# Kernel optimization log

Measured on AMD Instinct MI355X. Metric: run time of the kernel, lower is better.

Reference implementation:

```python
import jax, jax.numpy as jnp
import numpy as np

C = 1024            # hidden_dim // compression_rate
IN_DIM = 1024
OUT_DIM = 1024
FFT_LEN = C // 2 + 1
CURV = 1e-4         # self.c
EPS = 1e-7
LN_EPS = 1e-5


def _mobius_scalar_mul(r, x, c):
    # r (x) x = tanh(r * atanh(sqrt(c)||x||)) * x / (sqrt(c)||x||)
    sqrt_c = jnp.sqrt(c)
    norm = jnp.maximum(jnp.linalg.norm(x, axis=-1, keepdims=True), EPS)
    scn = jnp.clip(sqrt_c * norm, EPS, 1.0 - 1e-5)
    return jnp.tanh(r * jnp.arctanh(scn)) * x / (sqrt_c * norm)


def _mobius_add(x, y, c):
    x2 = jnp.sum(x * x, axis=-1, keepdims=True)
    y2 = jnp.sum(y * y, axis=-1, keepdims=True)
    xy = jnp.sum(x * y, axis=-1, keepdims=True)
    num = (1.0 + 2.0 * c * xy + c * y2) * x + (1.0 - c * x2) * y
    den = 1.0 + 2.0 * c * xy + (c * c) * x2 * y2
    return num / jnp.maximum(den, EPS)


def _poincare_ball_layer(u, v, c, t):
    # geodesic-style interpolation: ((1-t) (x) u) (+) (t (x) v)
    return _mobius_add(_mobius_scalar_mul(1.0 - t, u, c),
                       _mobius_scalar_mul(t, v, c), c)


def setup_inputs() -> dict:
    key = jax.random.key(0)
    k_x, k_p, k_d = jax.random.split(key, 3)
    std = 0.02
    x = jax.random.normal(k_x, (4, 2048, IN_DIM), dtype=jnp.float32)
    proj_w = jax.random.normal(k_p, (C, IN_DIM), dtype=jnp.float32) * std
    freq_w = jnp.zeros((FFT_LEN,), dtype=jnp.float32)
    t = jnp.float32(0.3)
    ln_g = jnp.ones((C,), dtype=jnp.float32)
    ln_b = jnp.zeros((C,), dtype=jnp.float32)
    down_w = jax.random.normal(k_d, (OUT_DIM, C), dtype=jnp.float32) * std
    scale = jnp.float32(1.0)
    return {"x": x, "proj_w": proj_w, "ln_g": ln_g, "ln_b": ln_b,
            "freq_w": freq_w, "t": t, "down_w": down_w, "scale": scale}


def reference(x, proj_w, ln_g, ln_b, freq_w, t, down_w, scale):
    B, L, _ = x.shape
    # non-sep branch (hidden_dim > in_dim): silu(Linear(x))
    comp = jax.nn.silu(jnp.einsum('bli,ci->blc', x, proj_w))
    mu = jnp.mean(comp, axis=-1, keepdims=True)
    var = jnp.var(comp, axis=-1, keepdims=True)
    comp = (comp - mu) * jax.lax.rsqrt(var + LN_EPS) * ln_g + ln_b
    comp = comp.reshape(-1, C)                     # [B*L, C]
    Xf = jnp.fft.rfft(comp, axis=1)                # [B*L, C//2+1]
    w = jax.nn.softmax(freq_w)[None, :]
    flat = jnp.fft.irfft(Xf * w, n=C, axis=1)
    flat = jnp.nan_to_num(flat)
    shift = jnp.nan_to_num(t * flat)
    hyp = jnp.nan_to_num(_poincare_ball_layer(flat, shift, CURV, t))
    hyp = hyp.reshape(B, L, C)
    return jnp.einsum('blc,oc->blo', hyp, down_w) * scale
```

## Files before the change

### kernel.cpp

```cpp
#include <hip/hip_runtime.h>
#include <math.h>

typedef float f32x4 __attribute__((ext_vector_type(4)));
typedef __bf16 bf16x8 __attribute__((ext_vector_type(8)));
typedef unsigned short u16x8 __attribute__((ext_vector_type(8)));

__device__ __forceinline__ unsigned short f2bf(float f) {
  unsigned u = __float_as_uint(f);
  unsigned r = (u + 0x7fffu + ((u >> 16) & 1u)) >> 16;
  return (unsigned short)r;
}
__device__ __forceinline__ float bf2f(unsigned short h) {
  return __uint_as_float(((unsigned)h) << 16);
}

__device__ __forceinline__ float blk_sum(float v, float* red, int tid) {
  #pragma unroll
  for (int o = 32; o; o >>= 1) v += __shfl_down(v, o);
  __syncthreads();
  if ((tid & 63) == 0) red[tid >> 6] = v;
  __syncthreads();
  return red[0] + red[1] + red[2] + red[3];
}

__global__ __launch_bounds__(256) void k_s(const float* __restrict__ fw,
                                           float* __restrict__ s,
                                           float* __restrict__ pw) {
  __shared__ float wsh[513];
  __shared__ float red[4];
  int tid = threadIdx.x;
  float m = -1e30f;
  for (int i = tid; i < 513; i += 256) m = fmaxf(m, fw[i]);
  #pragma unroll
  for (int o = 32; o; o >>= 1) m = fmaxf(m, __shfl_down(m, o));
  if ((tid & 63) == 0) red[tid >> 6] = m;
  __syncthreads();
  m = fmaxf(fmaxf(red[0], red[1]), fmaxf(red[2], red[3]));
  float sum = 0.f;
  for (int i = tid; i < 513; i += 256) {
    float e = expf(fw[i] - m);
    wsh[i] = e;
    sum += e;
  }
  sum = blk_sum(sum, red, tid);
  float inv = 1.f / sum;

  if (blockIdx.x == 0) {
    for (int i = tid; i < 513; i += 256) {
      float wn = wsh[i] * inv;
      float cf = (i == 0 || i == 512) ? 1.f : 2.f;
      pw[i] = cf * wn * wn * (1.f / 1024.f);
    }
  }

  int gid = blockIdx.x * 256 + tid;
  int d = gid >> 3;
  int chunk = gid & 7;
  float acc = 0.f;
  for (int f = 1 + chunk; f < 512; f += 8) {
    int p = (f * d) & 1023;
    acc += wsh[f] * __cosf(6.283185307179586f * (float)p * (1.f / 1024.f));
  }
  acc += __shfl_xor(acc, 1);
  acc += __shfl_xor(acc, 2);
  acc += __shfl_xor(acc, 4);
  if (chunk == 0) {
    float tot = wsh[0] + ((d & 1) ? -wsh[512] : wsh[512]) + 2.f * acc;
    s[d] = tot * inv * (1.f / 1024.f);
  }
}

__global__ __launch_bounds__(256) void k_prep(const float* __restrict__ x,
                                              const float* __restrict__ pw,
                                              const float* __restrict__ dw,
                                              const float* __restrict__ s,
                                              unsigned short* __restrict__ xb,
                                              unsigned short* __restrict__ pwb,
                                              unsigned short* __restrict__ dwb,
                                              unsigned short* __restrict__ Sb) {
  int b = blockIdx.x;
  int tid = threadIdx.x;
  if (b < 8192) {
    int i = b * 256 + tid;
    float4 v = ((const float4*)x)[i];
    ushort4 o;
    o.x = f2bf(v.x); o.y = f2bf(v.y); o.z = f2bf(v.z); o.w = f2bf(v.w);
    ((ushort4*)xb)[i] = o;
  } else if (b < 9216) {
    int i = (b - 8192) * 256 + tid;
    float4 v = ((const float4*)pw)[i];
    ushort4 o;
    o.x = f2bf(v.x); o.y = f2bf(v.y); o.z = f2bf(v.z); o.w = f2bf(v.w);
    ((ushort4*)pwb)[i] = o;
  } else if (b < 10240) {
    int i = (b - 9216) * 256 + tid;
    float4 v = ((const float4*)dw)[i];
    ushort4 o;
    o.x = f2bf(v.x); o.y = f2bf(v.y); o.z = f2bf(v.z); o.w = f2bf(v.w);
    ((ushort4*)dwb)[i] = o;
  } else {
    int idx = (b - 10240) * 256 + tid;
    int n = idx >> 8;
    int k0 = (idx & 255) * 4;
    ushort4 o;
    o.x = f2bf(s[(k0 + 0 - n) & 1023]);
    o.y = f2bf(s[(k0 + 1 - n) & 1023]);
    o.z = f2bf(s[(k0 + 2 - n) & 1023]);
    o.w = f2bf(s[(k0 + 3 - n) & 1023]);
    ((ushort4*)Sb)[idx] = o;
  }
}

__device__ __forceinline__ void gemm_body(const unsigned short* __restrict__ A,
                                          const unsigned short* __restrict__ B,
                                          int bm, int bn, int tid,
                                          char* AsB, char* BsB,
                                          f32x4 acc[4][4]) {
  const int lane = tid & 63;
  const int wave = tid >> 6;
  const int mhalf = (wave & 1) * 64;
  const int nhalf = (wave >> 1) * 64;
  const int ar = tid >> 3;
  const int ac = (((tid & 7) ^ (ar & 7))) * 8;
  const unsigned short* Abase = A + (size_t)(bm + ar) * 1024 + ac;
  const unsigned short* Bbase = B + (size_t)(bn + ar) * 1024 + ac;
  const int mrow = lane & 15;
  const int kq = lane >> 4;
  const int sw = mrow & 7;

  for (int kt = 0; kt < 16; ++kt) {
    const int k0 = kt * 64;
    #pragma unroll
    for (int r = 0; r < 4; ++r) {
      __builtin_amdgcn_global_load_lds(
          (const __attribute__((address_space(1))) void*)(Abase + (size_t)(r * 32) * 1024 + k0),
          (__attribute__((address_space(3))) void*)(AsB + r * 4096 + wave * 1024), 16, 0, 0);
      __builtin_amdgcn_global_load_lds(
          (const __attribute__((address_space(1))) void*)(Bbase + (size_t)(r * 32) * 1024 + k0),
          (__attribute__((address_space(3))) void*)(BsB + r * 4096 + wave * 1024), 16, 0, 0);
    }
    __syncthreads();
    #pragma unroll
    for (int kc = 0; kc < 2; ++kc) {
      const int chunk = (kc << 2) | kq;
      bf16x8 af[4], bfr[4];
      #pragma unroll
      for (int mt = 0; mt < 4; ++mt)
        af[mt] = *(const bf16x8*)(AsB + (mhalf + mt * 16 + mrow) * 128 + ((chunk ^ sw) << 4));
      #pragma unroll
      for (int nt = 0; nt < 4; ++nt)
        bfr[nt] = *(const bf16x8*)(BsB + (nhalf + nt * 16 + mrow) * 128 + ((chunk ^ sw) << 4));
      #pragma unroll
      for (int mt = 0; mt < 4; ++mt)
        #pragma unroll
        for (int nt = 0; nt < 4; ++nt)
          acc[mt][nt] = __builtin_amdgcn_mfma_f32_16x16x32_bf16(af[mt], bfr[nt], acc[mt][nt], 0, 0, 0);
    }
    __syncthreads();
  }
}

__global__ __launch_bounds__(256, 5) void k_gemm1w2(const unsigned short* __restrict__ xb,
                                                    const unsigned short* __restrict__ pwb,
                                                    const unsigned short* __restrict__ dwb,
                                                    const unsigned short* __restrict__ Sb,
                                                    unsigned short* __restrict__ comp,
                                                    unsigned short* __restrict__ W2) {
  __shared__ __align__(16) unsigned short As[128 * 64];
  __shared__ __align__(16) unsigned short Bs[64 * 64];
  const int tid = threadIdx.x;
  const int lane = tid & 63;
  const int wave = tid >> 6;
  const int mrow = lane & 15;
  const int kq = lane >> 4;
  const int sw = mrow & 7;
  char* AsB = (char*)As;
  char* BsB = (char*)Bs;

  if (blockIdx.x < 1024) {
    const int gid = blockIdx.x;
    const int xcd = gid & 7;
    const int j = gid >> 3;
    const int ntile = j & 15;
    const int bmIdx = xcd + 8 * (j >> 4);
    const int bm = bmIdx * 128;
    const int bn = ntile * 64;
    const int mhalf = (wave & 1) * 64;
    const int nhalf = (wave >> 1) * 32;
    f32x4 acc[4][2] = {};
    const int ar = tid >> 3;
    const int ac = (((tid & 7) ^ (ar & 7))) * 8;
    const unsigned short* Abase = xb + (size_t)(bm + ar) * 1024 + ac;
    const unsigned short* Bbase = pwb + (size_t)(bn + ar) * 1024 + ac;

    for (int kt = 0; kt < 16; ++kt) {
      const int k0 = kt * 64;
      #pragma unroll
      for (int r = 0; r < 4; ++r)
        __builtin_amdgcn_global_load_lds(
            (const __attribute__((address_space(1))) void*)(Abase + (size_t)(r * 32) * 1024 + k0),
            (__attribute__((address_space(3))) void*)(AsB + r * 4096 + wave * 1024), 16, 0, 0);
      #pragma unroll
      for (int r = 0; r < 2; ++r)
        __builtin_amdgcn_global_load_lds(
            (const __attribute__((address_space(1))) void*)(Bbase + (size_t)(r * 32) * 1024 + k0),
            (__attribute__((address_space(3))) void*)(BsB + r * 4096 + wave * 1024), 16, 0, 0);
      __syncthreads();
      #pragma unroll
      for (int kc = 0; kc < 2; ++kc) {
        const int chunk = (kc << 2) | kq;
        bf16x8 af[4], bfr[2];
        #pragma unroll
        for (int mt = 0; mt < 4; ++mt)
          af[mt] = *(const bf16x8*)(AsB + (mhalf + mt * 16 + mrow) * 128 + ((chunk ^ sw) << 4));
        #pragma unroll
        for (int nt = 0; nt < 2; ++nt)
          bfr[nt] = *(const bf16x8*)(BsB + (nhalf + nt * 16 + mrow) * 128 + ((chunk ^ sw) << 4));
        #pragma unroll
        for (int mt = 0; mt < 4; ++mt)
          #pragma unroll
          for (int nt = 0; nt < 2; ++nt)
            acc[mt][nt] = __builtin_amdgcn_mfma_f32_16x16x32_bf16(af[mt], bfr[nt], acc[mt][nt], 0, 0, 0);
      }
      __syncthreads();
    }

    const int col = bn + nhalf + (lane & 15);
    const int rbase = bm + mhalf + (lane >> 4) * 4;
    #pragma unroll
    for (int mt = 0; mt < 4; ++mt)
      #pragma unroll
      for (int r = 0; r < 4; ++r) {
        const int row = rbase + mt * 16 + r;
        #pragma unroll
        for (int nt = 0; nt < 2; ++nt) {
          float v = acc[mt][nt][r];
          comp[(size_t)row * 1024 + (col + nt * 16)] = f2bf(v / (1.f + expf(-v)));
        }
      }
    return;
  }

  const int wbid = blockIdx.x - 1024;
  const int bm = (wbid >> 4) * 64;
  const int bn = (wbid & 15) * 64;
  const int wm = wave & 1;
  const int wn = wave >> 1;
  f32x4 acc[2][2] = {};
  const int ar = tid >> 3;
  const int ac = (((tid & 7) ^ (ar & 7))) * 8;
  const unsigned short* Abase = dwb + (size_t)(bm + ar) * 1024 + ac;
  const unsigned short* Bbase = Sb + (size_t)(bn + ar) * 1024 + ac;
  for (int kt = 0; kt < 16; ++kt) {
    const int k0 = kt * 64;
    #pragma unroll
    for (int r = 0; r < 2; ++r) {
      __builtin_amdgcn_global_load_lds(
          (const __attribute__((address_space(1))) void*)(Abase + (size_t)(r * 32) * 1024 + k0),
          (__attribute__((address_space(3))) void*)(AsB + r * 4096 + wave * 1024), 16, 0, 0);
      __builtin_amdgcn_global_load_lds(
          (const __attribute__((address_space(1))) void*)(Bbase + (size_t)(r * 32) * 1024 + k0),
          (__attribute__((address_space(3))) void*)(BsB + r * 4096 + wave * 1024), 16, 0, 0);
    }
    __syncthreads();
    #pragma unroll
    for (int kc = 0; kc < 2; ++kc) {
      const int chunk = (kc << 2) | kq;
      bf16x8 af[2], bfr[2];
      #pragma unroll
      for (int mt = 0; mt < 2; ++mt)
        af[mt] = *(const bf16x8*)(AsB + (wm * 32 + mt * 16 + mrow) * 128 + ((chunk ^ sw) << 4));
      #pragma unroll
      for (int nt = 0; nt < 2; ++nt)
        bfr[nt] = *(const bf16x8*)(BsB + (wn * 32 + nt * 16 + mrow) * 128 + ((chunk ^ sw) << 4));
      #pragma unroll
      for (int mt = 0; mt < 2; ++mt)
        #pragma unroll
        for (int nt = 0; nt < 2; ++nt)
          acc[mt][nt] = __builtin_amdgcn_mfma_f32_16x16x32_bf16(af[mt], bfr[nt], acc[mt][nt], 0, 0, 0);
    }
    __syncthreads();
  }
  const int col = bn + wn * 32 + (lane & 15);
  const int rbase = bm + wm * 32 + (lane >> 4) * 4;
  #pragma unroll
  for (int mt = 0; mt < 2; ++mt)
    #pragma unroll
    for (int nt = 0; nt < 2; ++nt)
      #pragma unroll
      for (int r = 0; r < 4; ++r) {
        int row = rbase + mt * 16 + r;
        W2[(size_t)row * 1024 + (col + nt * 16)] = f2bf(acc[mt][nt][r]);
      }
}

#define BFLY(I, J, C, S)                                       \
  {                                                            \
    float tr_ = zr[J] * (C) - zi[J] * (S);                     \
    float ti_ = zr[J] * (S) + zi[J] * (C);                     \
    zr[J] = zr[I] - tr_; zi[J] = zi[I] - ti_;                  \
    zr[I] += tr_;        zi[I] += ti_;                         \
  }

__global__ __launch_bounds__(256) void k_ln(unsigned short* __restrict__ comp,
                                            const float* __restrict__ ln_g,
                                            const float* __restrict__ ln_b,
                                            const float* __restrict__ pw_par,
                                            float* __restrict__ u2) {
  const int tid = threadIdx.x;
  const int lane = tid & 63;
  const int wv = tid >> 6;
  const int row = blockIdx.x * 4 + wv;
  const size_t rowoff = (size_t)row * 1024;
  const int bl = __brev((unsigned)lane) >> 26;
  const int ybase = bl * 16;

  const u16x8* src = (const u16x8*)(comp + rowoff + ybase);
  u16x8 a0 = src[0], a1 = src[1];
  float y[16];
  #pragma unroll
  for (int i = 0; i < 8; ++i) { y[i] = bf2f(a0[i]); y[8 + i] = bf2f(a1[i]); }

  float s1 = 0.f;
  #pragma unroll
  for (int i = 0; i < 16; ++i) s1 += y[i];
  #pragma unroll
  for (int o = 32; o; o >>= 1) s1 += __shfl_xor(s1, o);
  const float mu = s1 * (1.f / 1024.f);
  float s2 = 0.f;
  #pragma unroll
  for (int i = 0; i < 16; ++i) { float d = y[i] - mu; s2 += d * d; }
  #pragma unroll
  for (int o = 32; o; o >>= 1) s2 += __shfl_xor(s2, o);
  const float inv = rsqrtf(s2 * (1.f / 1024.f) + 1e-5f);

  const float4* gp = (const float4*)(ln_g + ybase);
  const float4* bp = (const float4*)(ln_b + ybase);
  #pragma unroll
  for (int q = 0; q < 4; ++q) {
    float4 g = gp[q], b = bp[q];
    y[4 * q + 0] = (y[4 * q + 0] - mu) * inv * g.x + b.x;
    y[4 * q + 1] = (y[4 * q + 1] - mu) * inv * g.y + b.y;
    y[4 * q + 2] = (y[4 * q + 2] - mu) * inv * g.z + b.z;
    y[4 * q + 3] = (y[4 * q + 3] - mu) * inv * g.w + b.w;
  }
  u16x8 o0, o1;
  #pragma unroll
  for (int i = 0; i < 8; ++i) { o0[i] = f2bf(y[i]); o1[i] = f2bf(y[8 + i]); }
  u16x8* dst = (u16x8*)(comp + rowoff + ybase);
  dst[0] = o0; dst[1] = o1;

  float zr[8], zi[8];
  const int cmap[8] = {0, 4, 2, 6, 1, 5, 3, 7};
  #pragma unroll
  for (int r = 0; r < 8; ++r) { zr[r] = y[2 * cmap[r]]; zi[r] = y[2 * cmap[r] + 1]; }

  #pragma unroll
  for (int s = 1; s <= 6; ++s) {
    const int half = 1 << (s - 1);
    const int pos = lane & (half - 1);
    float c, sn;
    __sincosf(-3.14159265358979f * (float)pos / (float)half, &sn, &c);
    const bool hi = (lane & half) != 0;
    #pragma unroll
    for (int r = 0; r < 8; ++r) {
      const float pr = __shfl_xor(zr[r], half);
      const float pi = __shfl_xor(zi[r], half);
      const float ur = hi ? pr : zr[r];
      const float ui = hi ? pi : zi[r];
      const float vr = hi ? zr[r] : pr;
      const float vi = hi ? zi[r] : pi;
      const float tr = vr * c - vi * sn;
      const float ti = vr * sn + vi * c;
      zr[r] = hi ? (ur - tr) : (ur + tr);
      zi[r] = hi ? (ui - ti) : (ui + ti);
    }
  }
  {
    float c, sn;
    __sincosf(-3.14159265358979f * (float)lane * (1.f / 64.f), &sn, &c);
    BFLY(0, 1, c, sn); BFLY(2, 3, c, sn); BFLY(4, 5, c, sn); BFLY(6, 7, c, sn);
  }
  {
    float ca, sa, cb, sb;
    __sincosf(-3.14159265358979f * (float)lane * (1.f / 128.f), &sa, &ca);
    __sincosf(-3.14159265358979f * (float)(64 + lane) * (1.f / 128.f), &sb, &cb);
    BFLY(0, 2, ca, sa); BFLY(4, 6, ca, sa);
    BFLY(1, 3, cb, sb); BFLY(5, 7, cb, sb);
  }
  {
    float ca, sa, cb, sb, cc, sc, cd, sd;
    __sincosf(-3.14159265358979f * (float)lane * (1.f / 256.f), &sa, &ca);
    __sincosf(-3.14159265358979f * (float)(64 + lane) * (1.f / 256.f), &sb, &cb);
    __sincosf(-3.14159265358979f * (float)(128 + lane) * (1.f / 256.f), &sc, &cc);
    __sincosf(-3.14159265358979f * (float)(192 + lane) * (1.f / 256.f), &sd, &cd);
    BFLY(0, 4, ca, sa); BFLY(1, 5, cb, sb); BFLY(2, 6, cc, sc); BFLY(3, 7, cd, sd);
  }

  float partial = 0.f;
  const int srcl = (64 - lane) & 63;
  #pragma unroll
  for (int r = 0; r < 8; ++r) {
    const int k = r * 64 + lane;
    float mr = __shfl(zr[7 - r], srcl);
    float mi = __shfl(zi[7 - r], srcl);
    if (lane == 0) { mr = zr[(8 - r) & 7]; mi = zi[(8 - r) & 7]; }
    const float er = 0.5f * (zr[r] + mr);
    const float ei = 0.5f * (zi[r] - mi);
    const float orr = 0.5f * (zi[r] + mi);
    const float oi = -0.5f * (zr[r] - mr);
    float c, sn;
    __sincosf(-3.14159265358979f * (float)k * (1.f / 512.f), &sn, &c);
    const float xr = er + orr * c - oi * sn;
    const float xi = ei + orr * sn + oi * c;
    partial += pw_par[k] * (xr * xr + xi * xi);
  }
  if (lane == 0) {
    const float x512 = zr[0] - zi[0];
    partial += pw_par[512] * x512 * x512;
  }
  #pragma unroll
  for (int o = 32; o; o >>= 1) partial += __shfl_xor(partial, o);
  if (lane == 0) u2[row] = partial;
}

__device__ __forceinline__ float gamma_from_u2(float U2, float tv) {
  const float sc = 0.01f;
  const float c = 1e-4f;
  float nrm = sqrtf(U2);
  float nu = fmaxf(nrm, 1e-7f);
  float su = fminf(fmaxf(sc * nu, 1e-7f), 1.f - 1e-5f);
  float Af = tanhf((1.f - tv) * atanhf(su)) / (sc * nu);
  float nvn = fmaxf(fabsf(tv) * nrm, 1e-7f);
  float svv = fminf(fmaxf(sc * nvn, 1e-7f), 1.f - 1e-5f);
  float Bf = tv * tanhf(tv * atanhf(svv)) / (sc * nvn);
  float x2s = Af * Af * U2, y2s = Bf * Bf * U2, xys = Af * Bf * U2;
  float numc = (1.f + 2.f * c * xys + c * y2s) * Af + (1.f - c * x2s) * Bf;
  float den = fmaxf(1.f + 2.f * c * xys + c * c * x2s * y2s, 1e-7f);
  return numc / den;
}

__global__ __launch_bounds__(256, 4) void k_gemm23(const unsigned short* __restrict__ comp,
                                                   const unsigned short* __restrict__ W2,
                                                   const float* __restrict__ u2,
                                                   const float* __restrict__ t_ptr,
                                                   const float* __restrict__ scale_ptr,
                                                   float* __restrict__ out) {
  __shared__ __align__(16) unsigned short As[128 * 64];
  __shared__ __align__(16) unsigned short Bs[128 * 64];
  __shared__ float gs[128];
  const int tid = threadIdx.x;
  const int lane = tid & 63;
  const int wave = tid >> 6;
  const int xcd = blockIdx.x & 7;
  const int j = blockIdx.x >> 3;
  const int ntile = j & 7;
  const int bmIdx = xcd + 8 * (j >> 3);
  const int bm = bmIdx * 128;
  const int bn = ntile * 128;

  if (tid < 128) gs[tid] = gamma_from_u2(u2[bm + tid], t_ptr[0]) * scale_ptr[0];

  f32x4 acc[4][4] = {};
  gemm_body(comp, W2, bm, bn, tid, (char*)As, (char*)Bs, acc);

  const int col = bn + (wave >> 1) * 64 + (lane & 15);
  const int rbase = bm + (wave & 1) * 64 + (lane >> 4) * 4;
  #pragma unroll
  for (int mt = 0; mt < 4; ++mt)
    #pragma unroll
    for (int r = 0; r < 4; ++r) {
      const int row = rbase + mt * 16 + r;
      const float gsc = gs[row - bm];
      #pragma unroll
      for (int nt = 0; nt < 4; ++nt)
        out[(size_t)row * 1024 + (col + nt * 16)] = acc[mt][nt][r] * gsc;
    }
}

extern "C" void kernel_launch(void* const* d_in, const int* in_sizes, int n_in,
                              void* d_out, int out_size, void* d_ws, size_t ws_size,
                              hipStream_t stream) {
  const float* x      = (const float*)d_in[0];
  const float* proj_w = (const float*)d_in[1];
  const float* ln_g   = (const float*)d_in[2];
  const float* ln_b   = (const float*)d_in[3];
  const float* freq_w = (const float*)d_in[4];
  const float* t_p    = (const float*)d_in[5];
  const float* down_w = (const float*)d_in[6];
  const float* scale  = (const float*)d_in[7];

  char* ws = (char*)d_ws;
  unsigned short* xb   = (unsigned short*)ws;
  unsigned short* pwb  = (unsigned short*)(ws + (16u << 20));
  unsigned short* dwb  = (unsigned short*)(ws + (18u << 20));
  unsigned short* comp = (unsigned short*)(ws + (20u << 20));
  unsigned short* Sb   = (unsigned short*)(ws + (36u << 20));
  unsigned short* W2   = (unsigned short*)(ws + (38u << 20));
  float* s_buf         = (float*)(ws + (40u << 20));
  float* pw_par        = (float*)(ws + (40u << 20) + 4096);
  float* u2            = (float*)(ws + (40u << 20) + 8192);

  k_s<<<32, 256, 0, stream>>>(freq_w, s_buf, pw_par);
  k_prep<<<11264, 256, 0, stream>>>(x, proj_w, down_w, s_buf, xb, pwb, dwb, Sb);
  k_gemm1w2<<<1280, 256, 0, stream>>>(xb, pwb, dwb, Sb, comp, W2);
  k_ln<<<2048, 256, 0, stream>>>(comp, ln_g, ln_b, pw_par, u2);
  k_gemm23<<<512, 256, 0, stream>>>(comp, W2, u2, t_p, scale, (float*)d_out);
}
```

Before: 181.5 us.

## Double-buffer LDS tiles with async prefetch in all GEMM loops

```diff
diff --git a/kernel.cpp b/kernel.cpp
--- a/kernel.cpp
+++ b/kernel.cpp
@@ -111,71 +111,25 @@
   }
 }
 
-__device__ __forceinline__ void gemm_body(const unsigned short* __restrict__ A,
-                                          const unsigned short* __restrict__ B,
-                                          int bm, int bn, int tid,
-                                          char* AsB, char* BsB,
-                                          f32x4 acc[4][4]) {
-  const int lane = tid & 63;
-  const int wave = tid >> 6;
-  const int mhalf = (wave & 1) * 64;
-  const int nhalf = (wave >> 1) * 64;
-  const int ar = tid >> 3;
-  const int ac = (((tid & 7) ^ (ar & 7))) * 8;
-  const unsigned short* Abase = A + (size_t)(bm + ar) * 1024 + ac;
-  const unsigned short* Bbase = B + (size_t)(bn + ar) * 1024 + ac;
-  const int mrow = lane & 15;
-  const int kq = lane >> 4;
-  const int sw = mrow & 7;
-
-  for (int kt = 0; kt < 16; ++kt) {
-    const int k0 = kt * 64;
-    #pragma unroll
-    for (int r = 0; r < 4; ++r) {
-      __builtin_amdgcn_global_load_lds(
-          (const __attribute__((address_space(1))) void*)(Abase + (size_t)(r * 32) * 1024 + k0),
-          (__attribute__((address_space(3))) void*)(AsB + r * 4096 + wave * 1024), 16, 0, 0);
-      __builtin_amdgcn_global_load_lds(
-          (const __attribute__((address_space(1))) void*)(Bbase + (size_t)(r * 32) * 1024 + k0),
-          (__attribute__((address_space(3))) void*)(BsB + r * 4096 + wave * 1024), 16, 0, 0);
-    }
-    __syncthreads();
-    #pragma unroll
-    for (int kc = 0; kc < 2; ++kc) {
-      const int chunk = (kc << 2) | kq;
-      bf16x8 af[4], bfr[4];
-      #pragma unroll
-      for (int mt = 0; mt < 4; ++mt)
-        af[mt] = *(const bf16x8*)(AsB + (mhalf + mt * 16 + mrow) * 128 + ((chunk ^ sw) << 4));
-      #pragma unroll
-      for (int nt = 0; nt < 4; ++nt)
-        bfr[nt] = *(const bf16x8*)(BsB + (nhalf + nt * 16 + mrow) * 128 + ((chunk ^ sw) << 4));
-      #pragma unroll
-      for (int mt = 0; mt < 4; ++mt)
-        #pragma unroll
-        for (int nt = 0; nt < 4; ++nt)
-          acc[mt][nt] = __builtin_amdgcn_mfma_f32_16x16x32_bf16(af[mt], bfr[nt], acc[mt][nt], 0, 0, 0);
-    }
-    __syncthreads();
-  }
-}
-
-__global__ __launch_bounds__(256, 5) void k_gemm1w2(const unsigned short* __restrict__ xb,
+#define GB_BARRIER asm volatile("s_barrier" ::: "memory")
+#define GB_WAITV(N) asm volatile("s_waitcnt vmcnt(" #N ")" ::: "memory")
+
+__global__ __launch_bounds__(256, 3) void k_gemm1w2(const unsigned short* __restrict__ xb,
                                                     const unsigned short* __restrict__ pwb,
                                                     const unsigned short* __restrict__ dwb,
                                                     const unsigned short* __restrict__ Sb,
                                                     unsigned short* __restrict__ comp,
                                                     unsigned short* __restrict__ W2) {
-  __shared__ __align__(16) unsigned short As[128 * 64];
-  __shared__ __align__(16) unsigned short Bs[64 * 64];
+  __shared__ __align__(16) unsigned short As[2][128 * 64];
+  __shared__ __align__(16) unsigned short Bs[2][64 * 64];
   const int tid = threadIdx.x;
   const int lane = tid & 63;
   const int wave = tid >> 6;
   const int mrow = lane & 15;
   const int kq = lane >> 4;
   const int sw = mrow & 7;
-  char* AsB = (char*)As;
-  char* BsB = (char*)Bs;
+  const int ar = tid >> 3;
+  const int ac = (((tid & 7) ^ (ar & 7))) * 8;
 
   if (blockIdx.x < 1024) {
     const int gid = blockIdx.x;
@@ -188,42 +142,49 @@
     const int mhalf = (wave & 1) * 64;
     const int nhalf = (wave >> 1) * 32;
     f32x4 acc[4][2] = {};
-    const int ar = tid >> 3;
-    const int ac = (((tid & 7) ^ (ar & 7))) * 8;
     const unsigned short* Abase = xb + (size_t)(bm + ar) * 1024 + ac;
     const unsigned short* Bbase = pwb + (size_t)(bn + ar) * 1024 + ac;
 
-    for (int kt = 0; kt < 16; ++kt) {
-      const int k0 = kt * 64;
-      #pragma unroll
-      for (int r = 0; r < 4; ++r)
-        __builtin_amdgcn_global_load_lds(
-            (const __attribute__((address_space(1))) void*)(Abase + (size_t)(r * 32) * 1024 + k0),
-            (__attribute__((address_space(3))) void*)(AsB + r * 4096 + wave * 1024), 16, 0, 0);
-      #pragma unroll
-      for (int r = 0; r < 2; ++r)
-        __builtin_amdgcn_global_load_lds(
-            (const __attribute__((address_space(1))) void*)(Bbase + (size_t)(r * 32) * 1024 + k0),
-            (__attribute__((address_space(3))) void*)(BsB + r * 4096 + wave * 1024), 16, 0, 0);
-      __syncthreads();
-      #pragma unroll
-      for (int kc = 0; kc < 2; ++kc) {
-        const int chunk = (kc << 2) | kq;
-        bf16x8 af[4], bfr[2];
-        #pragma unroll
-        for (int mt = 0; mt < 4; ++mt)
-          af[mt] = *(const bf16x8*)(AsB + (mhalf + mt * 16 + mrow) * 128 + ((chunk ^ sw) << 4));
-        #pragma unroll
-        for (int nt = 0; nt < 2; ++nt)
-          bfr[nt] = *(const bf16x8*)(BsB + (nhalf + nt * 16 + mrow) * 128 + ((chunk ^ sw) << 4));
-        #pragma unroll
-        for (int mt = 0; mt < 4; ++mt)
-          #pragma unroll
-          for (int nt = 0; nt < 2; ++nt)
-            acc[mt][nt] = __builtin_amdgcn_mfma_f32_16x16x32_bf16(af[mt], bfr[nt], acc[mt][nt], 0, 0, 0);
-      }
-      __syncthreads();
+#define G1_STAGE(KT, BUF)                                                                     \
+    { const int k0_ = (KT) * 64;                                                              \
+      _Pragma("unroll")                                                                       \
+      for (int r = 0; r < 4; ++r)                                                             \
+        __builtin_amdgcn_global_load_lds(                                                     \
+            (const __attribute__((address_space(1))) void*)(Abase + (size_t)(r * 32) * 1024 + k0_), \
+            (__attribute__((address_space(3))) void*)((char*)As[BUF] + r * 4096 + wave * 1024), 16, 0, 0); \
+      _Pragma("unroll")                                                                       \
+      for (int r = 0; r < 2; ++r)                                                             \
+        __builtin_amdgcn_global_load_lds(                                                     \
+            (const __attribute__((address_space(1))) void*)(Bbase + (size_t)(r * 32) * 1024 + k0_), \
+            (__attribute__((address_space(3))) void*)((char*)Bs[BUF] + r * 4096 + wave * 1024), 16, 0, 0); }
+
+#define G1_COMP(BUF)                                                                          \
+    { const char* AsB = (const char*)As[BUF];                                                 \
+      const char* BsB = (const char*)Bs[BUF];                                                 \
+      _Pragma("unroll")                                                                       \
+      for (int kc = 0; kc < 2; ++kc) {                                                        \
+        const int chunk = (kc << 2) | kq;                                                     \
+        bf16x8 af[4], bfr[2];                                                                 \
+        _Pragma("unroll")                                                                     \
+        for (int mt = 0; mt < 4; ++mt)                                                        \
+          af[mt] = *(const bf16x8*)(AsB + (mhalf + mt * 16 + mrow) * 128 + ((chunk ^ sw) << 4)); \
+        _Pragma("unroll")                                                                     \
+        for (int nt = 0; nt < 2; ++nt)                                                        \
+          bfr[nt] = *(const bf16x8*)(BsB + (nhalf + nt * 16 + mrow) * 128 + ((chunk ^ sw) << 4)); \
+        _Pragma("unroll")                                                                     \
+        for (int mt = 0; mt < 4; ++mt)                                                        \
+          _Pragma("unroll")                                                                   \
+          for (int nt = 0; nt < 2; ++nt)                                                      \
+            acc[mt][nt] = __builtin_amdgcn_mfma_f32_16x16x32_bf16(af[mt], bfr[nt], acc[mt][nt], 0, 0, 0); } }
+
+    G1_STAGE(0, 0);
+    #pragma unroll 1
+    for (int kt = 0; kt < 14; kt += 2) {
+      G1_STAGE(kt + 1, 1); GB_WAITV(6); GB_BARRIER; G1_COMP(0); GB_BARRIER;
+      G1_STAGE(kt + 2, 0); GB_WAITV(6); GB_BARRIER; G1_COMP(1); GB_BARRIER;
     }
+    G1_STAGE(15, 1); GB_WAITV(6); GB_BARRIER; G1_COMP(0); GB_BARRIER;
+    GB_WAITV(0); GB_BARRIER; G1_COMP(1);
 
     const int col = bn + nhalf + (lane & 15);
     const int rbase = bm + mhalf + (lane >> 4) * 4;
@@ -247,40 +208,48 @@
   const int wm = wave & 1;
   const int wn = wave >> 1;
   f32x4 acc[2][2] = {};
-  const int ar = tid >> 3;
-  const int ac = (((tid & 7) ^ (ar & 7))) * 8;
   const unsigned short* Abase = dwb + (size_t)(bm + ar) * 1024 + ac;
   const unsigned short* Bbase = Sb + (size_t)(bn + ar) * 1024 + ac;
-  for (int kt = 0; kt < 16; ++kt) {
-    const int k0 = kt * 64;
-    #pragma unroll
-    for (int r = 0; r < 2; ++r) {
-      __builtin_amdgcn_global_load_lds(
-          (const __attribute__((address_space(1))) void*)(Abase + (size_t)(r * 32) * 1024 + k0),
-          (__attribute__((address_space(3))) void*)(AsB + r * 4096 + wave * 1024), 16, 0, 0);
-      __builtin_amdgcn_global_load_lds(
-          (const __attribute__((address_space(1))) void*)(Bbase + (size_t)(r * 32) * 1024 + k0),
-          (__attribute__((address_space(3))) void*)(BsB + r * 4096 + wave * 1024), 16, 0, 0);
-    }
-    __syncthreads();
-    #pragma unroll
-    for (int kc = 0; kc < 2; ++kc) {
-      const int chunk = (kc << 2) | kq;
-      bf16x8 af[2], bfr[2];
-      #pragma unroll
-      for (int mt = 0; mt < 2; ++mt)
-        af[mt] = *(const bf16x8*)(AsB + (wm * 32 + mt * 16 + mrow) * 128 + ((chunk ^ sw) << 4));
-      #pragma unroll
-      for (int nt = 0; nt < 2; ++nt)
-        bfr[nt] = *(const bf16x8*)(BsB + (wn * 32 + nt * 16 + mrow) * 128 + ((chunk ^ sw) << 4));
-      #pragma unroll
-      for (int mt = 0; mt < 2; ++mt)
-        #pragma unroll
-        for (int nt = 0; nt < 2; ++nt)
-          acc[mt][nt] = __builtin_amdgcn_mfma_f32_16x16x32_bf16(af[mt], bfr[nt], acc[mt][nt], 0, 0, 0);
-    }
-    __syncthreads();
-  }
+
+#define W2_STAGE(KT, BUF)                                                                     \
+  { const int k0_ = (KT) * 64;                                                                \
+    _Pragma("unroll")                                                                         \
+    for (int r = 0; r < 2; ++r) {                                                             \
+      __builtin_amdgcn_global_load_lds(                                                       \
+          (const __attribute__((address_space(1))) void*)(Abase + (size_t)(r * 32) * 1024 + k0_), \
+          (__attribute__((address_space(3))) void*)((char*)As[BUF] + r * 4096 + wave * 1024), 16, 0, 0); \
+      __builtin_amdgcn_global_load_lds(                                                       \
+          (const __attribute__((address_space(1))) void*)(Bbase + (size_t)(r * 32) * 1024 + k0_), \
+          (__attribute__((address_space(3))) void*)((char*)Bs[BUF] + r * 4096 + wave * 1024), 16, 0, 0); } }
+
+#define W2_COMP(BUF)                                                                          \
+  { const char* AsB = (const char*)As[BUF];                                                   \
+    const char* BsB = (const char*)Bs[BUF];                                                   \
+    _Pragma("unroll")                                                                         \
+    for (int kc = 0; kc < 2; ++kc) {                                                          \
+      const int chunk = (kc << 2) | kq;                                                       \
+      bf16x8 af[2], bfr[2];                                                                   \
+      _Pragma("unroll")                                                                       \
+      for (int mt = 0; mt < 2; ++mt)                                                          \
+        af[mt] = *(const bf16x8*)(AsB + (wm * 32 + mt * 16 + mrow) * 128 + ((chunk ^ sw) << 4)); \
+      _Pragma("unroll")                                                                       \
+      for (int nt = 0; nt < 2; ++nt)                                                          \
+        bfr[nt] = *(const bf16x8*)(BsB + (wn * 32 + nt * 16 + mrow) * 128 + ((chunk ^ sw) << 4)); \
+      _Pragma("unroll")                                                                       \
+      for (int mt = 0; mt < 2; ++mt)                                                          \
+        _Pragma("unroll")                                                                     \
+        for (int nt = 0; nt < 2; ++nt)                                                        \
+          acc[mt][nt] = __builtin_amdgcn_mfma_f32_16x16x32_bf16(af[mt], bfr[nt], acc[mt][nt], 0, 0, 0); } }
+
+  W2_STAGE(0, 0);
+  #pragma unroll 1
+  for (int kt = 0; kt < 14; kt += 2) {
+    W2_STAGE(kt + 1, 1); GB_WAITV(4); GB_BARRIER; W2_COMP(0); GB_BARRIER;
+    W2_STAGE(kt + 2, 0); GB_WAITV(4); GB_BARRIER; W2_COMP(1); GB_BARRIER;
+  }
+  W2_STAGE(15, 1); GB_WAITV(4); GB_BARRIER; W2_COMP(0); GB_BARRIER;
+  GB_WAITV(0); GB_BARRIER; W2_COMP(1);
+
   const int col = bn + wn * 32 + (lane & 15);
   const int rbase = bm + wm * 32 + (lane >> 4) * 4;
   #pragma unroll
@@ -440,14 +409,14 @@
   return numc / den;
 }
 
-__global__ __launch_bounds__(256, 4) void k_gemm23(const unsigned short* __restrict__ comp,
+__global__ __launch_bounds__(256, 2) void k_gemm23(const unsigned short* __restrict__ comp,
                                                    const unsigned short* __restrict__ W2,
                                                    const float* __restrict__ u2,
                                                    const float* __restrict__ t_ptr,
                                                    const float* __restrict__ scale_ptr,
                                                    float* __restrict__ out) {
-  __shared__ __align__(16) unsigned short As[128 * 64];
-  __shared__ __align__(16) unsigned short Bs[128 * 64];
+  __shared__ __align__(16) unsigned short As[2][128 * 64];
+  __shared__ __align__(16) unsigned short Bs[2][128 * 64];
   __shared__ float gs[128];
   const int tid = threadIdx.x;
   const int lane = tid & 63;
@@ -458,11 +427,58 @@
   const int bmIdx = xcd + 8 * (j >> 3);
   const int bm = bmIdx * 128;
   const int bn = ntile * 128;
+  const int mrow = lane & 15;
+  const int kq = lane >> 4;
+  const int sw = mrow & 7;
+  const int mhalf = (wave & 1) * 64;
+  const int nhalf = (wave >> 1) * 64;
+  const int ar = tid >> 3;
+  const int ac = (((tid & 7) ^ (ar & 7))) * 8;
+  const unsigned short* Abase = comp + (size_t)(bm + ar) * 1024 + ac;
+  const unsigned short* Bbase = W2 + (size_t)(bn + ar) * 1024 + ac;
 
   if (tid < 128) gs[tid] = gamma_from_u2(u2[bm + tid], t_ptr[0]) * scale_ptr[0];
 
   f32x4 acc[4][4] = {};
-  gemm_body(comp, W2, bm, bn, tid, (char*)As, (char*)Bs, acc);
+
+#define G3_STAGE(KT, BUF)                                                                     \
+  { const int k0_ = (KT) * 64;                                                                \
+    _Pragma("unroll")                                                                         \
+    for (int r = 0; r < 4; ++r) {                                                             \
+      __builtin_amdgcn_global_load_lds(                                                       \
+          (const __attribute__((address_space(1))) void*)(Abase + (size_t)(r * 32) * 1024 + k0_), \
+          (__attribute__((address_space(3))) void*)((char*)As[BUF] + r * 4096 + wave * 1024), 16, 0, 0); \
+      __builtin_amdgcn_global_load_lds(                                                       \
+          (const __attribute__((address_space(1))) void*)(Bbase + (size_t)(r * 32) * 1024 + k0_), \
+          (__attribute__((address_space(3))) void*)((char*)Bs[BUF] + r * 4096 + wave * 1024), 16, 0, 0); } }
+
+#define G3_COMP(BUF)                                                                          \
+  { const char* AsB = (const char*)As[BUF];                                                   \
+    const char* BsB = (const char*)Bs[BUF];                                                   \
+    _Pragma("unroll")                                                                         \
+    for (int kc = 0; kc < 2; ++kc) {                                                          \
+      const int chunk = (kc << 2) | kq;                                                       \
+      bf16x8 af[4], bfr[4];                                                                   \
+      _Pragma("unroll")                                                                       \
+      for (int mt = 0; mt < 4; ++mt)                                                          \
+        af[mt] = *(const bf16x8*)(AsB + (mhalf + mt * 16 + mrow) * 128 + ((chunk ^ sw) << 4)); \
+      _Pragma("unroll")                                                                       \
+      for (int nt = 0; nt < 4; ++nt)                                                          \
+        bfr[nt] = *(const bf16x8*)(BsB + (nhalf + nt * 16 + mrow) * 128 + ((chunk ^ sw) << 4)); \
+      _Pragma("unroll")                                                                       \
+      for (int mt = 0; mt < 4; ++mt)                                                          \
+        _Pragma("unroll")                                                                     \
+        for (int nt = 0; nt < 4; ++nt)                                                        \
+          acc[mt][nt] = __builtin_amdgcn_mfma_f32_16x16x32_bf16(af[mt], bfr[nt], acc[mt][nt], 0, 0, 0); } }
+
+  G3_STAGE(0, 0);
+  #pragma unroll 1
+  for (int kt = 0; kt < 14; kt += 2) {
+    G3_STAGE(kt + 1, 1); GB_WAITV(8); GB_BARRIER; G3_COMP(0); GB_BARRIER;
+    G3_STAGE(kt + 2, 0); GB_WAITV(8); GB_BARRIER; G3_COMP(1); GB_BARRIER;
+  }
+  G3_STAGE(15, 1); GB_WAITV(8); GB_BARRIER; G3_COMP(0); GB_BARRIER;
+  GB_WAITV(0); GB_BARRIER; G3_COMP(1);
 
   const int col = bn + (wave >> 1) * 64 + (lane & 15);
   const int rbase = bm + (wave & 1) * 64 + (lane >> 4) * 4;
```

New measurement: 180.9 us. Within noise of the previous version (-0.4%).
